# Kernel optimization log

Measured on AMD Instinct MI355X. Metric: run time of the kernel, lower is better.

The kernel has to match this reference:

```python
import jax, jax.numpy as jnp
import numpy as np

B, T, C, H = 2, 2048, 1024, 16
HS = C // H  # head_size = 64
EPS = 1e-5


def setup_inputs() -> dict:
    key = jax.random.key(0)
    ks = jax.random.split(key, 12)
    s = 0.02
    return {
        "x": jax.random.normal(ks[0], (B, T, C), jnp.float32),
        # per-head q/k/v linears stacked on a leading head axis [H, C, HS]
        "Wq": jax.random.normal(ks[1], (H, C, HS), jnp.float32) * s,
        "bq": jnp.zeros((H, HS), jnp.float32),
        "Wk": jax.random.normal(ks[2], (H, C, HS), jnp.float32) * s,
        "bk": jnp.zeros((H, HS), jnp.float32),
        "Wv": jax.random.normal(ks[3], (H, C, HS), jnp.float32) * s,
        "bv": jnp.zeros((H, HS), jnp.float32),
        # output projection [H*HS, C] == [C, C]
        "Wo": jax.random.normal(ks[4], (C, C), jnp.float32) * s,
        "bo": jnp.zeros((C,), jnp.float32),
        # feed-forward: C -> 4C -> C
        "W1": jax.random.normal(ks[5], (C, 4 * C), jnp.float32) * s,
        "b1": jnp.zeros((4 * C,), jnp.float32),
        "W2": jax.random.normal(ks[6], (4 * C, C), jnp.float32) * s,
        "b2": jnp.zeros((C,), jnp.float32),
        # custom LayerNorm params (broadcast over last dim)
        "gamma1": jnp.ones((C,), jnp.float32),
        "beta1": jnp.zeros((C,), jnp.float32),
        "gamma2": jnp.ones((C,), jnp.float32),
        "beta2": jnp.zeros((C,), jnp.float32),
    }


def _ln(x, gamma, beta):
    # NOTE: faithful to the source: normalizes over axis=1 (the SEQUENCE axis
    # for [B,T,C] input), uses unbiased variance (torch default), and puts eps
    # OUTSIDE the sqrt: (x - mean) / (sqrt(var) + eps).
    mean = x.mean(axis=1, keepdims=True)
    var = x.var(axis=1, keepdims=True, ddof=1)
    return gamma * ((x - mean) / (jnp.sqrt(var) + EPS)) + beta


def reference(x, Wq, bq, Wk, bk, Wv, bv, Wo, bo, W1, b1, W2, b2,
              gamma1, beta1, gamma2, beta2):
    # --- self-attention sublayer (pre-norm, residual) ---
    h = _ln(x, gamma1, beta1)
    q = jnp.einsum('btc,hcd->bhtd', h, Wq) + bq[None, :, None, :]
    k = jnp.einsum('btc,hcd->bhtd', h, Wk) + bk[None, :, None, :]
    v = jnp.einsum('btc,hcd->bhtd', h, Wv) + bv[None, :, None, :]
    wei = jax.nn.softmax(jnp.einsum('bhtd,bhsd->bhts', q, k) * (HS ** -0.5), axis=-1)
    attn = jnp.einsum('bhts,bhsd->bhtd', wei, v)          # [B,H,T,HS]
    attn = attn.transpose(0, 2, 1, 3).reshape(B, T, H * HS)  # head-order concat
    x = x + attn @ Wo + bo
    # --- feed-forward sublayer (pre-norm, residual) ---
    h2 = _ln(x, gamma2, beta2)
    x = x + jax.nn.relu(h2 @ W1 + b1) @ W2 + b2
    return x
```

## Files before the change

### kernel.cpp

```cpp
#include <hip/hip_runtime.h>
#include <hip/hip_bf16.h>

#define Bq 2
#define Tq 2048
#define Cq 1024
#define Hq 16
#define HSq 64
#define EPSq 1e-5f

using bf16 = __hip_bfloat16;
using f32x4 = __attribute__((ext_vector_type(4))) float;
using f32x16 = __attribute__((ext_vector_type(16))) float;
using bf16x8 = __attribute__((ext_vector_type(8))) __bf16;

__device__ __forceinline__ bf16 f2bf(float f) { return __float2bfloat16(f); }
__device__ __forceinline__ __bf16 f2n(float f) {
    return __builtin_bit_cast(__bf16, __float2bfloat16(f));
}
__device__ __forceinline__ unsigned short f2u(float f) {
    return __builtin_bit_cast(unsigned short, __float2bfloat16(f));
}
__device__ __forceinline__ void gload16(const void* g, void* l) {
    __builtin_amdgcn_global_load_lds((const __attribute__((address_space(1))) void*)g,
                                     (__attribute__((address_space(3))) void*)l, 16, 0, 0);
}

__global__ void k_transpose(const float* __restrict__ src, bf16* __restrict__ dst,
                            int R, int Cc, long strideSrc, long strideDst) {
    __shared__ bf16 tile[32][33];
    const long zb = blockIdx.z;
    src += zb * strideSrc;
    dst += zb * strideDst;
    int c0 = blockIdx.x * 32, r0 = blockIdx.y * 32;
    int tx = threadIdx.x & 31, ty = threadIdx.x >> 5;
    for (int i = ty; i < 32; i += 8)
        tile[i][tx] = f2bf(src[(long)(r0 + i) * Cc + (c0 + tx)]);
    __syncthreads();
    for (int i = ty; i < 32; i += 8)
        dst[(long)(c0 + i) * R + (r0 + tx)] = tile[tx][i];
}

__global__ void k_pack_bias(const float* __restrict__ a, const float* __restrict__ b,
                            const float* __restrict__ c, float* __restrict__ dst) {
    int i = blockIdx.x * 256 + threadIdx.x;
    dst[i] = a[i];
    dst[1024 + i] = b[i];
    dst[2048 + i] = c[i];
}

__global__ void k_ln_part(const float* __restrict__ x, float* __restrict__ ps,
                          float* __restrict__ pss) {
    int c = blockIdx.x * 256 + threadIdx.x;
    int b = blockIdx.y;
    int tc = blockIdx.z;
    const float* p = x + (long)b * Tq * Cq + (long)tc * 64 * Cq + c;
    float s = 0.f, ss = 0.f;
    for (int t = 0; t < 64; ++t) {
        float v = p[(long)t * Cq];
        s += v;
        ss += v * v;
    }
    long o = ((long)tc * Bq + b) * Cq + c;
    ps[o] = s;
    pss[o] = ss;
}

__global__ void k_ln_fin(const float* __restrict__ ps, const float* __restrict__ pss,
                         float* __restrict__ mean, float* __restrict__ rstd) {
    int i = blockIdx.x * 256 + threadIdx.x;
    float s = 0.f, ss = 0.f;
    for (int tc = 0; tc < 32; ++tc) {
        s += ps[(long)tc * (Bq * Cq) + i];
        ss += pss[(long)tc * (Bq * Cq) + i];
    }
    float m = s / (float)Tq;
    float var = (ss - s * m) / (float)(Tq - 1);
    var = fmaxf(var, 0.f);
    mean[i] = m;
    rstd[i] = 1.0f / (sqrtf(var) + EPSq);
}

__global__ void k_ln_apply(const float* __restrict__ x, const float* __restrict__ mean,
                           const float* __restrict__ rstd, const float* __restrict__ gamma,
                           const float* __restrict__ beta, bf16* __restrict__ out) {
    long i = (long)blockIdx.x * 256 + threadIdx.x;
    int c = (int)(i & (Cq - 1));
    long bt = i >> 10;
    int b = (int)(bt >> 11);
    float m = mean[b * Cq + c], r = rstd[b * Cq + c];
    out[i] = f2bf(gamma[c] * ((x[i] - m) * r) + beta[c]);
}

template <int MODE>
__global__ __launch_bounds__(256, 3) void k_gemm_nt(
    const bf16* __restrict__ A, int lda, const bf16* __restrict__ Bt, int ldb, int K,
    const float* __restrict__ bias, bf16* __restrict__ outB, int ldout) {
    __shared__ __bf16 sA[128 * 32];
    __shared__ __bf16 sB[128 * 32];
    const int m0 = blockIdx.y * 128, n0 = blockIdx.x * 128;
    const int tid = threadIdx.x;
    const int lane = tid & 63, wave = tid >> 6;
    const int lane15 = lane & 15, quad = lane >> 4;
    const int wm = (wave >> 1) * 64, wn = (wave & 1) * 64;
    const int srow = wave * 16 + (lane >> 2);
    const int scol = (lane & 3) * 8;
    __bf16* ldsA0 = &sA[wave * 512];
    __bf16* ldsA1 = &sA[2048 + wave * 512];
    __bf16* ldsB0 = &sB[wave * 512];
    __bf16* ldsB1 = &sB[2048 + wave * 512];
    const bf16* Ap = A + (long)(m0 + srow) * lda + scol;
    const bf16* Ap2 = Ap + 64L * lda;
    const bf16* Bp = Bt + (long)(n0 + srow) * ldb + scol;
    const bf16* Bp2 = Bp + 64L * ldb;

    f32x4 acc[4][4];
#pragma unroll
    for (int i = 0; i < 4; ++i)
#pragma unroll
        for (int j = 0; j < 4; ++j)
#pragma unroll
            for (int p = 0; p < 4; ++p) acc[i][j][p] = 0.f;

    for (int k0 = 0; k0 < K; k0 += 32) {
        __syncthreads();
        gload16(Ap + k0, ldsA0);
        gload16(Ap2 + k0, ldsA1);
        gload16(Bp + k0, ldsB0);
        gload16(Bp2 + k0, ldsB1);
        __syncthreads();
        bf16x8 af[4], bfr[4];
#pragma unroll
        for (int i = 0; i < 4; ++i)
            af[i] = *(const bf16x8*)(&sA[(wm + i * 16 + lane15) * 32 + quad * 8]);
#pragma unroll
        for (int j = 0; j < 4; ++j)
            bfr[j] = *(const bf16x8*)(&sB[(wn + j * 16 + lane15) * 32 + quad * 8]);
#pragma unroll
        for (int i = 0; i < 4; ++i)
#pragma unroll
            for (int j = 0; j < 4; ++j)
                acc[i][j] =
                    __builtin_amdgcn_mfma_f32_16x16x32_bf16(af[i], bfr[j], acc[i][j], 0, 0, 0);
    }
    if (MODE == 0) {
#pragma unroll
        for (int i = 0; i < 4; ++i) {
            const int mm = m0 + wm + i * 16 + quad * 4;
            const int b = mm >> 11, t4 = mm & (Tq - 1);
#pragma unroll
            for (int j = 0; j < 4; ++j) {
                const int n = n0 + wn + j * 16 + lane15;
                const int which = n >> 10, hh = (n >> 6) & (Hq - 1), d = n & (HSq - 1);
                const long bh = (long)b * Hq + hh;
                const float bb = bias[n];
                if (which == 0) {
#pragma unroll
                    for (int p = 0; p < 4; ++p)
                        outB[bh * 131072 + (long)(t4 + p) * HSq + d] =
                            f2bf((acc[i][j][p] + bb) * 0.125f);
                } else if (which == 1) {
#pragma unroll
                    for (int p = 0; p < 4; ++p)
                        outB[4194304L + bh * 131072 + (long)(t4 + p) * HSq + d] =
                            f2bf(acc[i][j][p] + bb);
                } else {
                    ushort4 pk;
                    pk.x = f2u(acc[i][j][0] + bb);
                    pk.y = f2u(acc[i][j][1] + bb);
                    pk.z = f2u(acc[i][j][2] + bb);
                    pk.w = f2u(acc[i][j][3] + bb);
                    *(ushort4*)(&outB[8388608L + bh * 131072 + (long)d * Tq + t4]) = pk;
                }
            }
        }
    } else {
#pragma unroll
        for (int i = 0; i < 4; ++i) {
#pragma unroll
            for (int p = 0; p < 4; ++p) {
                const int m = m0 + wm + i * 16 + quad * 4 + p;
#pragma unroll
                for (int j = 0; j < 4; ++j) {
                    const int n = n0 + wn + j * 16 + lane15;
                    outB[(long)m * ldout + n] = f2bf(fmaxf(acc[i][j][p] + bias[n], 0.f));
                }
            }
        }
    }
}

template <int MODE>
__global__ __launch_bounds__(256, 4) void k_gemm_n64(
    const bf16* __restrict__ A, int lda, const bf16* __restrict__ Bt, int ldb, int K,
    const float* __restrict__ bias, const float* __restrict__ residF,
    float* __restrict__ outF, int ldout) {
    __shared__ __bf16 sA[128 * 32];
    __shared__ __bf16 sB[64 * 32];
    const int m0 = blockIdx.y * 128, n0 = blockIdx.x * 64;
    const int tid = threadIdx.x;
    const int lane = tid & 63, wave = tid >> 6;
    const int lane15 = lane & 15, quad = lane >> 4;
    const int wm = wave * 32;
    const int srow = wave * 16 + (lane >> 2);
    const int scol = (lane & 3) * 8;
    __bf16* ldsA0 = &sA[wave * 512];
    __bf16* ldsA1 = &sA[2048 + wave * 512];
    __bf16* ldsB0 = &sB[wave * 512];
    const bf16* Ap = A + (long)(m0 + srow) * lda + scol;
    const bf16* Ap2 = Ap + 64L * lda;
    const bf16* Bp = Bt + (long)(n0 + srow) * ldb + scol;

    f32x4 acc[2][4];
#pragma unroll
    for (int i = 0; i < 2; ++i)
#pragma unroll
        for (int j = 0; j < 4; ++j)
#pragma unroll
            for (int p = 0; p < 4; ++p) acc[i][j][p] = 0.f;

    for (int k0 = 0; k0 < K; k0 += 32) {
        __syncthreads();
        gload16(Ap + k0, ldsA0);
        gload16(Ap2 + k0, ldsA1);
        gload16(Bp + k0, ldsB0);
        __syncthreads();
        bf16x8 af[2], bfr[4];
#pragma unroll
        for (int i = 0; i < 2; ++i)
            af[i] = *(const bf16x8*)(&sA[(wm + i * 16 + lane15) * 32 + quad * 8]);
#pragma unroll
        for (int j = 0; j < 4; ++j)
            bfr[j] = *(const bf16x8*)(&sB[(j * 16 + lane15) * 32 + quad * 8]);
#pragma unroll
        for (int i = 0; i < 2; ++i)
#pragma unroll
            for (int j = 0; j < 4; ++j)
                acc[i][j] =
                    __builtin_amdgcn_mfma_f32_16x16x32_bf16(af[i], bfr[j], acc[i][j], 0, 0, 0);
    }
#pragma unroll
    for (int i = 0; i < 2; ++i) {
#pragma unroll
        for (int p = 0; p < 4; ++p) {
            const int m = m0 + wm + i * 16 + quad * 4 + p;
#pragma unroll
            for (int j = 0; j < 4; ++j) {
                const int n = n0 + j * 16 + lane15;
                outF[(long)m * ldout + n] =
                    acc[i][j][p] + bias[n] + residF[(long)m * ldout + n];
            }
        }
    }
}

__global__ __launch_bounds__(256, 4) void k_attn(const bf16* __restrict__ qkv,
                                                 bf16* __restrict__ attn) {
    __shared__ __bf16 sK[64 * 72];
    __shared__ __bf16 sVt[64 * 72];
    __shared__ __bf16 sP[4][32 * 72];
    const int bh = blockIdx.y;
    const int q0 = blockIdx.x * 128;
    const int tid = threadIdx.x, wave = tid >> 6, lane = tid & 63;
    const int lane31 = lane & 31, laneh = lane >> 5;
    const bf16* Qp = qkv + (long)bh * 131072;
    const bf16* Kp = qkv + 4194304L + (long)bh * 131072;
    const bf16* Vtp = qkv + 8388608L + (long)bh * 131072;
    bf16x8 qa[4];
#pragma unroll
    for (int s = 0; s < 4; ++s)
        qa[s] = *(const bf16x8*)(&Qp[(long)(q0 + wave * 32 + lane31) * HSq + s * 16 + laneh * 8]);
    f32x16 o[2];
#pragma unroll
    for (int dt = 0; dt < 2; ++dt)
#pragma unroll
        for (int r = 0; r < 16; ++r) o[dt][r] = 0.f;
    float rs[16];
#pragma unroll
    for (int r = 0; r < 16; ++r) rs[r] = 0.f;
    const int r0 = tid >> 3, c0 = (tid & 7) * 8;
    const int r1 = r0 + 32;

    for (int kc = 0; kc < Tq; kc += 64) {
        __syncthreads();
        *(uint4*)(&sK[r0 * 72 + c0]) = *(const uint4*)(&Kp[(long)(kc + r0) * HSq + c0]);
        *(uint4*)(&sK[r1 * 72 + c0]) = *(const uint4*)(&Kp[(long)(kc + r1) * HSq + c0]);
        *(uint4*)(&sVt[r0 * 72 + c0]) = *(const uint4*)(&Vtp[(long)r0 * Tq + kc + c0]);
        *(uint4*)(&sVt[r1 * 72 + c0]) = *(const uint4*)(&Vtp[(long)r1 * Tq + kc + c0]);
        __syncthreads();
#pragma unroll
        for (int nt = 0; nt < 2; ++nt) {
            f32x16 z;
#pragma unroll
            for (int r = 0; r < 16; ++r) z[r] = 0.f;
#pragma unroll
            for (int s = 0; s < 4; ++s) {
                bf16x8 kb =
                    *(const bf16x8*)(&sK[(nt * 32 + lane31) * 72 + s * 16 + laneh * 8]);
                z = __builtin_amdgcn_mfma_f32_32x32x16_bf16(qa[s], kb, z, 0, 0, 0);
            }
#pragma unroll
            for (int r = 0; r < 16; ++r) {
                float e = __expf(z[r]);
                rs[r] += e;
                const int row = (r & 3) + 8 * (r >> 2) + 4 * laneh;
                sP[wave][row * 72 + nt * 32 + lane31] = f2n(e);
            }
        }
        bf16x8 pa[4];
#pragma unroll
        for (int s = 0; s < 4; ++s)
            pa[s] = *(const bf16x8*)(&sP[wave][lane31 * 72 + s * 16 + laneh * 8]);
#pragma unroll
        for (int dt = 0; dt < 2; ++dt)
#pragma unroll
            for (int s = 0; s < 4; ++s) {
                bf16x8 vb =
                    *(const bf16x8*)(&sVt[(dt * 32 + lane31) * 72 + s * 16 + laneh * 8]);
                o[dt] = __builtin_amdgcn_mfma_f32_32x32x16_bf16(pa[s], vb, o[dt], 0, 0, 0);
            }
    }
    const int b = bh >> 4, hh = bh & 15;
#pragma unroll
    for (int r = 0; r < 16; ++r) {
        float v = rs[r];
        v += __shfl_xor(v, 1);
        v += __shfl_xor(v, 2);
        v += __shfl_xor(v, 4);
        v += __shfl_xor(v, 8);
        v += __shfl_xor(v, 16);
        float inv = 1.0f / v;
        const int row = (r & 3) + 8 * (r >> 2) + 4 * laneh;
        const int t = q0 + wave * 32 + row;
        const long base = ((long)b * Tq + t) * Cq + hh * HSq;
#pragma unroll
        for (int dt = 0; dt < 2; ++dt)
            attn[base + dt * 32 + lane31] = f2bf(o[dt][r] * inv);
    }
}

extern "C" void kernel_launch(void* const* d_in, const int* in_sizes, int n_in,
                              void* d_out, int out_size, void* d_ws, size_t ws_size,
                              hipStream_t stream) {
    const float* x = (const float*)d_in[0];
    const float* Wq = (const float*)d_in[1];
    const float* bqv = (const float*)d_in[2];
    const float* Wk = (const float*)d_in[3];
    const float* bkv = (const float*)d_in[4];
    const float* Wv = (const float*)d_in[5];
    const float* bvv = (const float*)d_in[6];
    const float* Wo = (const float*)d_in[7];
    const float* bo = (const float*)d_in[8];
    const float* W1 = (const float*)d_in[9];
    const float* b1 = (const float*)d_in[10];
    const float* W2 = (const float*)d_in[11];
    const float* b2 = (const float*)d_in[12];
    const float* g1 = (const float*)d_in[13];
    const float* be1 = (const float*)d_in[14];
    const float* g2 = (const float*)d_in[15];
    const float* be2 = (const float*)d_in[16];

    char* ws = (char*)d_ws;
    size_t off = 0;
    auto alloc = [&](size_t bytes) {
        void* p = ws + off;
        off += (bytes + 255) & ~(size_t)255;
        return p;
    };
    bf16* regA = (bf16*)alloc(32L * 1024 * 1024);
    float* x2 = (float*)alloc(4096L * 1024 * 4);
    bf16* buf1 = (bf16*)alloc(4096L * 1024 * 2);
    float* bqkv = (float*)alloc(3072L * 4);
    float* ps = (float*)alloc(32L * Bq * Cq * 4);
    float* pss = (float*)alloc(32L * Bq * Cq * 4);
    float* mean1 = (float*)alloc(Bq * Cq * 4);
    float* rstd1 = (float*)alloc(Bq * Cq * 4);
    float* mean2 = (float*)alloc(Bq * Cq * 4);
    float* rstd2 = (float*)alloc(Bq * Cq * 4);
    bf16* dres = (bf16*)d_out;
    float* outF = (float*)d_out;

    k_ln_part<<<dim3(4, Bq, 32), 256, 0, stream>>>(x, ps, pss);
    k_ln_fin<<<dim3(8), 256, 0, stream>>>(ps, pss, mean1, rstd1);
    k_ln_apply<<<dim3(16384), 256, 0, stream>>>(x, mean1, rstd1, g1, be1, dres);

    k_transpose<<<dim3(2, 32, 16), 256, 0, stream>>>(Wq, buf1, 1024, 64, 65536, 65536);
    k_transpose<<<dim3(2, 32, 16), 256, 0, stream>>>(Wk, buf1 + 1048576, 1024, 64, 65536, 65536);
    k_transpose<<<dim3(2, 32, 16), 256, 0, stream>>>(Wv, buf1 + 2097152, 1024, 64, 65536, 65536);
    k_pack_bias<<<dim3(4), 256, 0, stream>>>(bqv, bkv, bvv, bqkv);
    k_gemm_nt<0><<<dim3(24, 32), 256, 0, stream>>>(dres, 1024, buf1, 1024, 1024, bqkv, regA, 0);
    k_attn<<<dim3(16, 32), 256, 0, stream>>>(regA, dres);
    k_transpose<<<dim3(32, 32, 1), 256, 0, stream>>>(Wo, buf1, 1024, 1024, 0, 0);
    k_gemm_n64<1><<<dim3(16, 32), 256, 0, stream>>>(dres, 1024, buf1, 1024, 1024, bo, x, x2,
                                                    1024);
    k_ln_part<<<dim3(4, Bq, 32), 256, 0, stream>>>(x2, ps, pss);
    k_ln_fin<<<dim3(8), 256, 0, stream>>>(ps, pss, mean2, rstd2);
    k_ln_apply<<<dim3(16384), 256, 0, stream>>>(x2, mean2, rstd2, g2, be2, dres);

    k_transpose<<<dim3(128, 32, 1), 256, 0, stream>>>(W1, buf1, 1024, 4096, 0, 0);
    k_gemm_nt<2><<<dim3(32, 32), 256, 0, stream>>>(dres, 1024, buf1, 1024, 1024, b1, regA, 4096);
    k_transpose<<<dim3(32, 128, 1), 256, 0, stream>>>(W2, buf1, 4096, 1024, 0, 0);
    k_gemm_n64<3><<<dim3(16, 32), 256, 0, stream>>>(regA, 4096, buf1, 4096, 4096, b2, x2, outF,
                                                    1024);
}
```

Baseline: 434.9 us.

## Keep softmax probabilities in registers via transposed QK MFMA and register-prefetch K/V

The QK^T MFMA operands are swapped so each lane holds the scores for one query column. Exponentials are then packed to bf16 and exchanged across half-waves with shuffles to form the PV A-operand directly, which removes the per-wave LDS staging buffer for P and its write/read round trip. The row sum becomes a single scalar per lane and is reduced with one cross-half shuffle. The next K/V tile is also prefetched into registers while the current tile is computed, and launch bounds are relaxed to 2 blocks per SM, which allows more registers but may lower occupancy.

Measured after the change: 406.2 us. -6.6%, faster.

```diff
diff --git a/kernel.cpp b/kernel.cpp
--- a/kernel.cpp
+++ b/kernel.cpp
@@ -14,9 +14,6 @@
 using bf16x8 = __attribute__((ext_vector_type(8))) __bf16;
 
 __device__ __forceinline__ bf16 f2bf(float f) { return __float2bfloat16(f); }
-__device__ __forceinline__ __bf16 f2n(float f) {
-    return __builtin_bit_cast(__bf16, __float2bfloat16(f));
-}
 __device__ __forceinline__ unsigned short f2u(float f) {
     return __builtin_bit_cast(unsigned short, __float2bfloat16(f));
 }
@@ -253,11 +250,10 @@
     }
 }
 
-__global__ __launch_bounds__(256, 4) void k_attn(const bf16* __restrict__ qkv,
+__global__ __launch_bounds__(256, 2) void k_attn(const bf16* __restrict__ qkv,
                                                  bf16* __restrict__ attn) {
     __shared__ __bf16 sK[64 * 72];
     __shared__ __bf16 sVt[64 * 72];
-    __shared__ __bf16 sP[4][32 * 72];
     const int bh = blockIdx.y;
     const int q0 = blockIdx.x * 128;
     const int tid = threadIdx.x, wave = tid >> 6, lane = tid & 63;
@@ -274,19 +270,28 @@
     for (int dt = 0; dt < 2; ++dt)
 #pragma unroll
         for (int r = 0; r < 16; ++r) o[dt][r] = 0.f;
-    float rs[16];
-#pragma unroll
-    for (int r = 0; r < 16; ++r) rs[r] = 0.f;
+    float rs = 0.f;
     const int r0 = tid >> 3, c0 = (tid & 7) * 8;
     const int r1 = r0 + 32;
 
+    uint4 nk0 = *(const uint4*)(&Kp[(long)r0 * HSq + c0]);
+    uint4 nk1 = *(const uint4*)(&Kp[(long)r1 * HSq + c0]);
+    uint4 nv0 = *(const uint4*)(&Vtp[(long)r0 * Tq + c0]);
+    uint4 nv1 = *(const uint4*)(&Vtp[(long)r1 * Tq + c0]);
+
     for (int kc = 0; kc < Tq; kc += 64) {
         __syncthreads();
-        *(uint4*)(&sK[r0 * 72 + c0]) = *(const uint4*)(&Kp[(long)(kc + r0) * HSq + c0]);
-        *(uint4*)(&sK[r1 * 72 + c0]) = *(const uint4*)(&Kp[(long)(kc + r1) * HSq + c0]);
-        *(uint4*)(&sVt[r0 * 72 + c0]) = *(const uint4*)(&Vtp[(long)r0 * Tq + kc + c0]);
-        *(uint4*)(&sVt[r1 * 72 + c0]) = *(const uint4*)(&Vtp[(long)r1 * Tq + kc + c0]);
-        __syncthreads();
+        *(uint4*)(&sK[r0 * 72 + c0]) = nk0;
+        *(uint4*)(&sK[r1 * 72 + c0]) = nk1;
+        *(uint4*)(&sVt[r0 * 72 + c0]) = nv0;
+        *(uint4*)(&sVt[r1 * 72 + c0]) = nv1;
+        __syncthreads();
+        if (kc + 64 < Tq) {
+            nk0 = *(const uint4*)(&Kp[(long)(kc + 64 + r0) * HSq + c0]);
+            nk1 = *(const uint4*)(&Kp[(long)(kc + 64 + r1) * HSq + c0]);
+            nv0 = *(const uint4*)(&Vtp[(long)r0 * Tq + kc + 64 + c0]);
+            nv1 = *(const uint4*)(&Vtp[(long)r1 * Tq + kc + 64 + c0]);
+        }
 #pragma unroll
         for (int nt = 0; nt < 2; ++nt) {
             f32x16 z;
@@ -296,41 +301,54 @@
             for (int s = 0; s < 4; ++s) {
                 bf16x8 kb =
                     *(const bf16x8*)(&sK[(nt * 32 + lane31) * 72 + s * 16 + laneh * 8]);
-                z = __builtin_amdgcn_mfma_f32_32x32x16_bf16(qa[s], kb, z, 0, 0, 0);
-            }
+                z = __builtin_amdgcn_mfma_f32_32x32x16_bf16(kb, qa[s], z, 0, 0, 0);
+            }
+            float e[16];
 #pragma unroll
             for (int r = 0; r < 16; ++r) {
-                float e = __expf(z[r]);
-                rs[r] += e;
-                const int row = (r & 3) + 8 * (r >> 2) + 4 * laneh;
-                sP[wave][row * 72 + nt * 32 + lane31] = f2n(e);
+                e[r] = __expf(z[r]);
+                rs += e[r];
+            }
+            unsigned int pk[8];
+#pragma unroll
+            for (int g = 0; g < 4; ++g)
+#pragma unroll
+                for (int h = 0; h < 2; ++h)
+                    pk[g * 2 + h] = (unsigned int)f2u(e[g * 4 + 2 * h]) |
+                                    ((unsigned int)f2u(e[g * 4 + 2 * h + 1]) << 16);
+            unsigned int sa0 = laneh ? pk[0] : pk[2], sa1 = laneh ? pk[1] : pk[3];
+            unsigned int ra0 = __shfl_xor((int)sa0, 32), ra1 = __shfl_xor((int)sa1, 32);
+            unsigned int sb0 = laneh ? pk[4] : pk[6], sb1 = laneh ? pk[5] : pk[7];
+            unsigned int rb0 = __shfl_xor((int)sb0, 32), rb1 = __shfl_xor((int)sb1, 32);
+            uint4 f0, f1;
+            if (laneh == 0) {
+                f0 = {pk[0], pk[1], ra0, ra1};
+                f1 = {pk[4], pk[5], rb0, rb1};
+            } else {
+                f0 = {ra0, ra1, pk[2], pk[3]};
+                f1 = {rb0, rb1, pk[6], pk[7]};
+            }
+            bf16x8 pa0 = __builtin_bit_cast(bf16x8, f0);
+            bf16x8 pa1 = __builtin_bit_cast(bf16x8, f1);
+#pragma unroll
+            for (int dt = 0; dt < 2; ++dt) {
+                bf16x8 vb0 =
+                    *(const bf16x8*)(&sVt[(dt * 32 + lane31) * 72 + nt * 32 + laneh * 8]);
+                bf16x8 vb1 = *(const bf16x8*)(&sVt[(dt * 32 + lane31) * 72 + nt * 32 + 16 +
+                                                   laneh * 8]);
+                o[dt] = __builtin_amdgcn_mfma_f32_32x32x16_bf16(pa0, vb0, o[dt], 0, 0, 0);
+                o[dt] = __builtin_amdgcn_mfma_f32_32x32x16_bf16(pa1, vb1, o[dt], 0, 0, 0);
             }
         }
-        bf16x8 pa[4];
-#pragma unroll
-        for (int s = 0; s < 4; ++s)
-            pa[s] = *(const bf16x8*)(&sP[wave][lane31 * 72 + s * 16 + laneh * 8]);
-#pragma unroll
-        for (int dt = 0; dt < 2; ++dt)
-#pragma unroll
-            for (int s = 0; s < 4; ++s) {
-                bf16x8 vb =
-                    *(const bf16x8*)(&sVt[(dt * 32 + lane31) * 72 + s * 16 + laneh * 8]);
-                o[dt] = __builtin_amdgcn_mfma_f32_32x32x16_bf16(pa[s], vb, o[dt], 0, 0, 0);
-            }
-    }
+    }
+    float ltot = rs + __shfl_xor(rs, 32);
+    float linv = 1.0f / ltot;
     const int b = bh >> 4, hh = bh & 15;
 #pragma unroll
     for (int r = 0; r < 16; ++r) {
-        float v = rs[r];
-        v += __shfl_xor(v, 1);
-        v += __shfl_xor(v, 2);
-        v += __shfl_xor(v, 4);
-        v += __shfl_xor(v, 8);
-        v += __shfl_xor(v, 16);
-        float inv = 1.0f / v;
-        const int row = (r & 3) + 8 * (r >> 2) + 4 * laneh;
-        const int t = q0 + wave * 32 + row;
+        const int tl = (r & 3) + 8 * (r >> 2) + 4 * laneh;
+        float inv = __shfl(linv, tl);
+        const int t = q0 + wave * 32 + tl;
         const long base = ((long)b * Tq + t) * Cq + hh * HSq;
 #pragma unroll
         for (int dt = 0; dt < 2; ++dt)
```
